# Kernel tuning notes

Hardware: AMD Instinct MI355X
Metric: run time of the kernel (lower is better)

Reference implementation:

```python
import jax, jax.numpy as jnp
import numpy as np

B, R, H, W = 128, 8, 256, 256


def _conv(x, w, b):
    # x: [1, C_in, h, w], w: [C_out, C_in, 3, 3]; stride 2, pad 1, then bias + ReLU
    y = jax.lax.conv_general_dilated(
        x, w, window_strides=(2, 2), padding=((1, 1), (1, 1)),
        dimension_numbers=('NCHW', 'OIHW', 'NCHW'))
    return jax.nn.relu(y + b[None, :, None, None])


def _single(x, w1, b1, w2, b2, w3, b3, fw, fb):
    # x: [3, H, W]; one sample through its region's CNN expert
    h = x[None]                      # [1,3,H,W]
    h = _conv(h, w1, b1)             # [1,32,H/2,W/2]
    h = _conv(h, w2, b2)             # [1,64,H/4,W/4]
    h = _conv(h, w3, b3)             # [1,128,H/8,W/8]
    feat = h.mean(axis=(2, 3))[0]    # [128] global average pool
    return fw @ feat + fb            # [num_classes]


def setup_inputs() -> dict:
    key = jax.random.key(0)
    ks = jax.random.split(key, 10)
    s = 0.05
    return {
        'image': jax.random.normal(ks[0], (B, 3, H, W), jnp.float32),
        'region': jax.random.randint(ks[1], (B,), 0, R, jnp.int64),
        'w1': jax.random.normal(ks[2], (R, 32, 3, 3, 3), jnp.float32) * s,
        'b1': jax.random.normal(ks[3], (R, 32), jnp.float32) * s,
        'w2': jax.random.normal(ks[4], (R, 64, 32, 3, 3), jnp.float32) * s,
        'b2': jax.random.normal(ks[5], (R, 64), jnp.float32) * s,
        'w3': jax.random.normal(ks[6], (R, 128, 64, 3, 3), jnp.float32) * s,
        'b3': jax.random.normal(ks[7], (R, 128), jnp.float32) * s,
        'fw': jax.random.normal(ks[8], (R, 2, 128), jnp.float32) * s,
        'fb': jax.random.normal(ks[9], (R, 2), jnp.float32) * s,
    }


def reference(image, region, w1, b1, w2, b2, w3, b3, fw, fb):
    # MoE-style dispatch: gather each sample's region weights, vmap per-sample expert.
    r = region.astype(jnp.int32)
    pw = [jnp.take(p, r, axis=0) for p in (w1, b1, w2, b2, w3, b3, fw, fb)]
    out = jax.vmap(_single)(image, *pw)  # [B, num_classes]
    return out
```

## Files before the change

kernel.cpp:

```cpp
#include <hip/hip_runtime.h>
#include <cstdint>


typedef __attribute__((ext_vector_type(8))) short short8;
typedef __attribute__((ext_vector_type(4))) float floatx4;
typedef __attribute__((ext_vector_type(4))) unsigned short ushort4v;
typedef __attribute__((ext_vector_type(4))) float float4v;

__device__ inline unsigned short f2bf(float f) {
  union { float f; unsigned u; } x;
  x.f = f;
  unsigned u = x.u;
  u += 0x7FFFu + ((u >> 16) & 1u);
  return (unsigned short)(u >> 16);
}

__device__ inline void g2l16(const unsigned short* g, unsigned short* l) {
  __builtin_amdgcn_global_load_lds(
      (const __attribute__((address_space(1))) unsigned int*)g,
      (__attribute__((address_space(3))) unsigned int*)(unsigned int)(uintptr_t)l,
      16, 0, 0);
}

__global__ __launch_bounds__(128) void prep_k(const int* __restrict__ rp,
                                              int* __restrict__ rout,
                                              float* __restrict__ feat) {
  __shared__ int is64;
  if (threadIdx.x == 0) {
    int odd_or = 0;
    for (int i = 0; i < 64; ++i) odd_or |= rp[2 * i + 1];
    is64 = (odd_or == 0) ? 1 : 0;
  }
  __syncthreads();
  int b = threadIdx.x;
  int r = is64 ? rp[2 * b] : rp[b];
  rout[b] = r & 7;
  float* fr = feat + b * 128;
  for (int j = 0; j < 128; ++j) fr[j] = 0.f;
}

__global__ __launch_bounds__(256) void pack1_k(const float* __restrict__ w,
                                               unsigned short* __restrict__ dst) {
  int t = blockIdx.x * blockDim.x + threadIdx.x;
  if (t >= 16384) return;
  int j = t & 7, lane = (t >> 3) & 63, mt = (t >> 9) & 1, kg = (t >> 10) & 1,
      r = t >> 11;
  int oc = mt * 16 + (lane & 15);
  int q = (lane >> 4) & 3;
  int row = kg * 2 + (q >> 1);
  int idx = (q & 1) * 8 + j;
  int kx = idx >> 2, c = idx & 3;
  float val = 0.f;
  if (row < 3 && kx < 3 && c < 3) val = w[((r * 32 + oc) * 3 + c) * 9 + row * 3 + kx];
  dst[t] = f2bf(val);
}

template <int OC, int IC, int SUBK, int MTG>
__global__ __launch_bounds__(256) void packT_k(const float* __restrict__ w,
                                               unsigned short* __restrict__ dst) {
  const int total = 8 * 9 * SUBK * MTG * 512;
  int t = blockIdx.x * blockDim.x + threadIdx.x;
  if (t >= total) return;
  int j = t & 7, lane = (t >> 3) & 63;
  int u = t >> 9;
  int mt = u % MTG; u /= MTG;
  int s = u % SUBK; u /= SUBK;
  int tap = u % 9;
  int r = u / 9;
  int oc = mt * 16 + (lane & 15);
  int ic = s * 32 + ((lane >> 4) & 3) * 8 + j;
  dst[t] = f2bf(w[((r * OC + oc) * IC + ic) * 9 + tap]);
}

__global__ __launch_bounds__(256) void halo8_k(unsigned short* __restrict__ buf,
                                               int nplane, int HP, int WP) {
  int per = 2 * WP + 2 * (HP - 2);
  int t = blockIdx.x * blockDim.x + threadIdx.x;
  if (t >= nplane * per) return;
  int s = t / per, i = t - s * per;
  int y, x;
  if (i < WP) { y = 0; x = i; }
  else if (i < 2 * WP) { y = HP - 1; x = i - WP; }
  else {
    int ii = i - 2 * WP;
    y = 1 + (ii >> 1);
    x = (ii & 1) ? (WP - 1) : 0;
  }
  short8 z = {0, 0, 0, 0, 0, 0, 0, 0};
  *(short8*)(buf + ((size_t)s * HP * WP + y * WP + x) * 8) = z;
}

__global__ __launch_bounds__(256, 3) void conv12_k(
    const float* __restrict__ img, const unsigned short* __restrict__ w1p,
    const float* __restrict__ b1, const unsigned short* __restrict__ w2p,
    const float* __restrict__ b2, const int* __restrict__ rgn,
    unsigned short* __restrict__ outp, int b0) {
  __shared__ unsigned short imgT[11 * 168 * 4];
  __shared__ unsigned short h1T[9 * 4 * 66 * 8];
  __shared__ float sB1[32];
  __shared__ float sB2[64];
  const int tid = threadIdx.x;
  const int xh = blockIdx.x;
  const int oy0 = blockIdx.y * 4;
  const int bl = blockIdx.z;
  const int r = __builtin_amdgcn_readfirstlane(rgn[b0 + bl]);
  if (tid < 32) sB1[tid] = b1[r * 32 + tid];
  if (tid >= 64 && tid < 128) sB2[tid - 64] = b2[r * 64 + (tid - 64)];
  const float* ib = img + (size_t)(b0 + bl) * 3 * 65536;
  const int padx = xh ? 65 : 0;
  const bool skiptop = (oy0 == 0);
  const int rb = xh * 128 - 4;

  const int n = tid & 15, q = (tid >> 4) & 3, wv = tid >> 6;
  const int lane = tid & 63;
  const short8* wpb1 = (const short8*)w1p + (size_t)r * 256 + lane;
  short8 afr1[2][2];
#pragma unroll
  for (int kg = 0; kg < 2; ++kg)
#pragma unroll
    for (int m = 0; m < 2; ++m) afr1[kg][m] = wpb1[(kg * 2 + m) * 64];

  auto STAGE = [&](int t0, int nrows) {
    const int nch = nrows * 41;
    for (int seg = 0; seg < nch; seg += 256) {
      int c = seg + tid;
      if (c < nch) {
        int i = c / 41, cq = c - i * 41;
        int rv = 4 * oy0 - 3 + t0 + i;
        int cb = rb + 4 * cq;
        unsigned short* dp = &imgT[((size_t)i * 168 + (4 * cq - 1)) * 4];
        if (rv >= 0 && cq > 0 && cb >= 0 && cb + 3 <= 255) {
          const float* p = ib + (size_t)rv * 256 + cb;
          float4v a = *(const float4v*)p;
          float4v bb = *(const float4v*)(p + 65536);
          float4v cc = *(const float4v*)(p + 131072);
#pragma unroll
          for (int e = 0; e < 4; ++e) {
            ushort4v v = {f2bf(a[e]), f2bf(bb[e]), f2bf(cc[e]), 0};
            *(ushort4v*)(dp + e * 4) = v;
          }
        } else {
          for (int e = (cq == 0 ? 1 : 0); e < 4; ++e) {
            int cc2 = cb + e;
            ushort4v v = {0, 0, 0, 0};
            if (rv >= 0 && cc2 >= 0 && cc2 <= 255) {
              const float* p = ib + (size_t)rv * 256 + cc2;
              v.x = f2bf(p[0]);
              v.y = f2bf(p[65536]);
              v.z = f2bf(p[131072]);
            }
            *(ushort4v*)(dp + e * 4) = v;
          }
        }
      }
    }
  };

  auto CONV1ROW = [&](int hy, int phaseB) {
    floatx4 a1[5][2];
#pragma unroll
    for (int nt = 0; nt < 5; ++nt)
#pragma unroll
      for (int m = 0; m < 2; ++m) a1[nt][m] = (floatx4){0.f, 0.f, 0.f, 0.f};
#pragma unroll
    for (int kg = 0; kg < 2; ++kg) {
      int row = kg * 2 + (q >> 1);
      int rowc = (row < 3) ? row : 0;
      int tr = 2 * hy + rowc;
      int slot = phaseB ? (tr >= 11 ? tr - 11 : tr) : tr;
#pragma unroll
      for (int nt = 0; nt < 5; ++nt) {
        int lx = nt * 16 + n;
        short8 bfr = *(const short8*)&imgT[((size_t)slot * 168 + 2 * lx) * 4 +
                                           (q & 1) * 8];
#pragma unroll
        for (int m = 0; m < 2; ++m)
          a1[nt][m] = __builtin_amdgcn_mfma_f32_16x16x32_bf16(
              afr1[kg][m], bfr, a1[nt][m], 0, 0, 0);
      }
    }
#pragma unroll
    for (int nt = 0; nt < 5; ++nt) {
      int lx = nt * 16 + n;
      bool ok = (lx <= 65) && (lx != padx) && !(skiptop && hy == 0);
      if (ok) {
#pragma unroll
        for (int m = 0; m < 2; ++m) {
          ushort4v st;
#pragma unroll
          for (int rr = 0; rr < 4; ++rr) {
            float v = a1[nt][m][rr] + sB1[m * 16 + q * 4 + rr];
            st[rr] = f2bf(v > 0.f ? v : 0.f);
          }
          int cg = m * 2 + (q >> 1);
          *(ushort4v*)&h1T[(((size_t)hy * 4 + cg) * 66 + lx) * 8 +
                           (q & 1) * 4] = st;
        }
      }
    }
  };

  STAGE(0, 11);
  {
    short8 z8 = {0, 0, 0, 0, 0, 0, 0, 0};
    if (tid < 36) {
      int hy = tid / 4, cg = tid % 4;
      *(short8*)&h1T[(((size_t)hy * 4 + cg) * 66 + padx) * 8] = z8;
    }
    if (skiptop) {
      for (int c = tid; c < 264; c += 256) {
        int cg = c / 66, x = c - cg * 66;
        *(short8*)&h1T[(((size_t)0 * 4 + cg) * 66 + x) * 8] = z8;
      }
    }
  }
  __syncthreads();

  for (int hy = wv; hy <= 4; hy += 4) CONV1ROW(hy, 0);
  __syncthreads();

  STAGE(11, 8);
  __syncthreads();

  CONV1ROW(5 + wv, 1);
  __syncthreads();

  const short8* wpb2 = (const short8*)w2p + (size_t)r * 9 * 4 * 64 + lane;
  floatx4 a2[2][4];
#pragma unroll
  for (int nt = 0; nt < 2; ++nt)
#pragma unroll
    for (int m = 0; m < 4; ++m) a2[nt][m] = (floatx4){0.f, 0.f, 0.f, 0.f};
#pragma unroll
  for (int tap = 0; tap < 9; ++tap) {
    const int ky = tap / 3, kx = tap % 3;
    short8 af[4];
#pragma unroll
    for (int m = 0; m < 4; ++m) af[m] = wpb2[(tap * 4 + m) * 64];
    short8 bf[2];
#pragma unroll
    for (int nt = 0; nt < 2; ++nt) {
      int ox = nt * 16 + n;
      bf[nt] = *(const short8*)&h1T[((((2 * wv + ky) << 2) + q) * 66 +
                                    (2 * ox + kx)) * 8];
    }
#pragma unroll
    for (int m = 0; m < 4; ++m)
#pragma unroll
      for (int nt = 0; nt < 2; ++nt)
        a2[nt][m] = __builtin_amdgcn_mfma_f32_16x16x32_bf16(af[m], bf[nt],
                                                            a2[nt][m], 0, 0, 0);
  }
  unsigned short* ob = outp + (size_t)bl * 8 * 66 * 66 * 8;
  const int oy = oy0 + wv;
#pragma unroll
  for (int nt = 0; nt < 2; ++nt) {
    int ox = xh * 32 + nt * 16 + n;
#pragma unroll
    for (int m = 0; m < 4; ++m) {
      ushort4v st;
#pragma unroll
      for (int rr = 0; rr < 4; ++rr) {
        float v = a2[nt][m][rr] + sB2[m * 16 + q * 4 + rr];
        st[rr] = f2bf(v > 0.f ? v : 0.f);
      }
      int cg = m * 2 + (q >> 1);
      *(ushort4v*)&ob[(((size_t)cg * 66 + oy + 1) * 66 + ox + 1) * 8 +
                      (q & 1) * 4] = st;
    }
  }
}

__global__ __launch_bounds__(128, 2) void conv3lds_k(
    const unsigned short* __restrict__ in, const unsigned short* __restrict__ wp,
    const float* __restrict__ bias, const int* __restrict__ rgn,
    float* __restrict__ feat, int b0) {
  __shared__ unsigned short tile[9 * 4 * 66 * 8];
  __shared__ float sBias[128];
  __shared__ float sGap[2 * 128];
  const int tid = threadIdx.x;
  const int bl = blockIdx.y;
  const int b = b0 + bl;
  const int r = __builtin_amdgcn_readfirstlane(rgn[b]);
  sBias[tid] = bias[r * 128 + tid];
  const int oy0 = blockIdx.x * 4;
  const unsigned short* gbase = in + (size_t)bl * 8 * 66 * 66 * 8;
  const int lane = tid & 63, wv = tid >> 6;
  const int n = lane & 15, q = (lane >> 4) & 3;
  const short8* wpb = (const short8*)wp + (size_t)r * 9 * 2 * 8 * 64 + lane;
  floatx4 acc[4][8];
#pragma unroll
  for (int nt = 0; nt < 4; ++nt)
#pragma unroll
    for (int m = 0; m < 8; ++m) acc[nt][m] = (floatx4){0.f, 0.f, 0.f, 0.f};
#pragma unroll
  for (int s = 0; s < 2; ++s) {
    __syncthreads();
    for (int seg = 0; seg < 2376; seg += 128) {
      int c = seg + tid;
      if (c < 2376) {
        int iy = c / 264;
        int rem = c - iy * 264;
        int c8 = rem / 66;
        int x = rem - c8 * 66;
        const unsigned short* gp =
            gbase + (((size_t)(s * 4 + c8) * 66 + 2 * oy0 + iy) * 66 + x) * 8;
        g2l16(gp, tile + (size_t)(seg + wv * 64) * 8);
      }
    }
    __syncthreads();
#pragma unroll
    for (int tap = 0; tap < 9; ++tap) {
      const int ky = tap / 3, kx = tap % 3;
      short8 afr[8];
#pragma unroll
      for (int m = 0; m < 8; ++m) afr[m] = wpb[((tap * 2 + s) * 8 + m) * 64];
      short8 bfr[4];
#pragma unroll
      for (int nt = 0; nt < 4; ++nt) {
        int oyl = 2 * wv + (nt >> 1);
        int ox = ((nt & 1) << 4) + n;
        bfr[nt] = *(const short8*)&tile[(((2 * oyl + ky) * 4 + q) * 66 +
                                        (2 * ox + kx)) * 8];
      }
#pragma unroll
      for (int m = 0; m < 8; ++m)
#pragma unroll
        for (int nt = 0; nt < 4; ++nt)
          acc[nt][m] = __builtin_amdgcn_mfma_f32_16x16x32_bf16(afr[m], bfr[nt],
                                                               acc[nt][m], 0, 0, 0);
    }
  }
#pragma unroll
  for (int m = 0; m < 8; ++m)
#pragma unroll
    for (int rr = 0; rr < 4; ++rr) {
      float bv = sBias[m * 16 + q * 4 + rr];
      float vs = 0.f;
#pragma unroll
      for (int nt = 0; nt < 4; ++nt) {
        float v = acc[nt][m][rr] + bv;
        vs += (v > 0.f ? v : 0.f);
      }
      vs += __shfl_xor(vs, 1, 16);
      vs += __shfl_xor(vs, 2, 16);
      vs += __shfl_xor(vs, 4, 16);
      vs += __shfl_xor(vs, 8, 16);
      if (n == 0) sGap[wv * 128 + m * 16 + q * 4 + rr] = vs;
    }
  __syncthreads();
  atomicAdd(&feat[b * 128 + tid], sGap[tid] + sGap[128 + tid]);
}

__global__ __launch_bounds__(256) void head_k(
    const float* __restrict__ feat, const float* __restrict__ fw,
    const float* __restrict__ fb, const int* __restrict__ rgn,
    float* __restrict__ out) {
  int t = threadIdx.x;
  int b = t >> 1, c = t & 1;
  int r = rgn[b];
  const float* fwr = fw + (r * 2 + c) * 128;
  const float* fv = feat + b * 128;
  float a = 0.f;
#pragma unroll 8
  for (int j = 0; j < 128; ++j) a = fmaf(fwr[j], fv[j], a);
  out[t] = a * (1.0f / 1024.0f) + fb[r * 2 + c];
}

extern "C" void kernel_launch(void* const* d_in, const int* in_sizes, int n_in,
                              void* d_out, int out_size, void* d_ws, size_t ws_size,
                              hipStream_t stream) {
  const float* img = (const float*)d_in[0];
  const int* rgn_raw = (const int*)d_in[1];
  const float* w1 = (const float*)d_in[2];
  const float* b1 = (const float*)d_in[3];
  const float* w2 = (const float*)d_in[4];
  const float* b2 = (const float*)d_in[5];
  const float* w3 = (const float*)d_in[6];
  const float* b3 = (const float*)d_in[7];
  const float* fw = (const float*)d_in[8];
  const float* fb = (const float*)d_in[9];
  float* out = (float*)d_out;

  const size_t h2p_s = (size_t)8 * 66 * 66 * 8 * 2;
  const size_t per_sample = h2p_s;
  const size_t fixed = (size_t)16384 * 2 + (size_t)147456 * 2 +
                       (size_t)589824 * 2 + 128 * 128 * 4 + 512 + 16 * 256;
  int C = 128;
  while (C > 1 && fixed + (size_t)C * per_sample > ws_size) C >>= 1;

  char* ws = (char*)d_ws;
  size_t off = 0;
  auto alloc = [&](size_t bytes) {
    char* p = ws + off;
    off += (bytes + 255) & ~(size_t)255;
    return p;
  };
  unsigned short* h2p = (unsigned short*)alloc((size_t)C * h2p_s);
  unsigned short* w1p = (unsigned short*)alloc((size_t)16384 * 2);
  unsigned short* w2p = (unsigned short*)alloc((size_t)147456 * 2);
  unsigned short* w3p = (unsigned short*)alloc((size_t)589824 * 2);
  float* feat = (float*)alloc((size_t)128 * 128 * 4);
  int* rgn = (int*)alloc((size_t)128 * 4);

  hipLaunchKernelGGL(prep_k, dim3(1), dim3(128), 0, stream, rgn_raw, rgn, feat);
  hipLaunchKernelGGL(pack1_k, dim3(64), dim3(256), 0, stream, w1, w1p);
  hipLaunchKernelGGL((packT_k<64, 32, 1, 4>), dim3(576), dim3(256), 0, stream, w2, w2p);
  hipLaunchKernelGGL((packT_k<128, 64, 2, 8>), dim3(2304), dim3(256), 0, stream, w3, w3p);
  {
    int n2 = C * 8 * (2 * 66 + 2 * 64);
    hipLaunchKernelGGL(halo8_k, dim3((n2 + 255) / 256), dim3(256), 0, stream,
                       h2p, C * 8, 66, 66);
  }

  for (int b0 = 0; b0 < 128; b0 += C) {
    hipLaunchKernelGGL(conv12_k, dim3(2, 16, C), dim3(256), 0, stream,
                       img, w1p, b1, w2p, b2, rgn, h2p, b0);
    hipLaunchKernelGGL(conv3lds_k, dim3(8, C), dim3(128), 0, stream,
                       h2p, w3p, b3, rgn, feat, b0);
  }
  hipLaunchKernelGGL(head_k, dim3(1), dim3(256), 0, stream, feat, fw, fb, rgn, out);
}
```

Before: 287.1 us.

## Merge setup kernels into one launch and widen conv3 to 4 waves

```diff
diff --git a/kernel.cpp b/kernel.cpp
--- a/kernel.cpp
+++ b/kernel.cpp
@@ -22,72 +22,79 @@
       16, 0, 0);
 }
 
-__global__ __launch_bounds__(128) void prep_k(const int* __restrict__ rp,
-                                              int* __restrict__ rout,
-                                              float* __restrict__ feat) {
-  __shared__ int is64;
-  if (threadIdx.x == 0) {
-    int odd_or = 0;
-    for (int i = 0; i < 64; ++i) odd_or |= rp[2 * i + 1];
-    is64 = (odd_or == 0) ? 1 : 0;
-  }
-  __syncthreads();
-  int b = threadIdx.x;
-  int r = is64 ? rp[2 * b] : rp[b];
-  rout[b] = r & 7;
-  float* fr = feat + b * 128;
-  for (int j = 0; j < 128; ++j) fr[j] = 0.f;
-}
-
-__global__ __launch_bounds__(256) void pack1_k(const float* __restrict__ w,
-                                               unsigned short* __restrict__ dst) {
-  int t = blockIdx.x * blockDim.x + threadIdx.x;
-  if (t >= 16384) return;
-  int j = t & 7, lane = (t >> 3) & 63, mt = (t >> 9) & 1, kg = (t >> 10) & 1,
-      r = t >> 11;
-  int oc = mt * 16 + (lane & 15);
-  int q = (lane >> 4) & 3;
-  int row = kg * 2 + (q >> 1);
-  int idx = (q & 1) * 8 + j;
-  int kx = idx >> 2, c = idx & 3;
-  float val = 0.f;
-  if (row < 3 && kx < 3 && c < 3) val = w[((r * 32 + oc) * 3 + c) * 9 + row * 3 + kx];
-  dst[t] = f2bf(val);
-}
-
-template <int OC, int IC, int SUBK, int MTG>
-__global__ __launch_bounds__(256) void packT_k(const float* __restrict__ w,
-                                               unsigned short* __restrict__ dst) {
-  const int total = 8 * 9 * SUBK * MTG * 512;
-  int t = blockIdx.x * blockDim.x + threadIdx.x;
-  if (t >= total) return;
-  int j = t & 7, lane = (t >> 3) & 63;
-  int u = t >> 9;
-  int mt = u % MTG; u /= MTG;
-  int s = u % SUBK; u /= SUBK;
-  int tap = u % 9;
-  int r = u / 9;
-  int oc = mt * 16 + (lane & 15);
-  int ic = s * 32 + ((lane >> 4) & 3) * 8 + j;
-  dst[t] = f2bf(w[((r * OC + oc) * IC + ic) * 9 + tap]);
-}
-
-__global__ __launch_bounds__(256) void halo8_k(unsigned short* __restrict__ buf,
-                                               int nplane, int HP, int WP) {
-  int per = 2 * WP + 2 * (HP - 2);
-  int t = blockIdx.x * blockDim.x + threadIdx.x;
-  if (t >= nplane * per) return;
-  int s = t / per, i = t - s * per;
-  int y, x;
-  if (i < WP) { y = 0; x = i; }
-  else if (i < 2 * WP) { y = HP - 1; x = i - WP; }
-  else {
-    int ii = i - 2 * WP;
-    y = 1 + (ii >> 1);
-    x = (ii & 1) ? (WP - 1) : 0;
-  }
-  short8 z = {0, 0, 0, 0, 0, 0, 0, 0};
-  *(short8*)(buf + ((size_t)s * HP * WP + y * WP + x) * 8) = z;
+__global__ __launch_bounds__(256) void setup_k(
+    const int* __restrict__ rp, int* __restrict__ rout, float* __restrict__ feat,
+    const float* __restrict__ w1, unsigned short* __restrict__ w1p,
+    const float* __restrict__ w2, unsigned short* __restrict__ w2p,
+    const float* __restrict__ w3, unsigned short* __restrict__ w3p,
+    unsigned short* __restrict__ h2p, int nhalo) {
+  const int tid = threadIdx.x;
+  if (blockIdx.x == 0) {
+    __shared__ int is64;
+    if (tid == 0) {
+      int odd_or = 0;
+      for (int i = 0; i < 64; ++i) odd_or |= rp[2 * i + 1];
+      is64 = (odd_or == 0) ? 1 : 0;
+    }
+    __syncthreads();
+    if (tid < 128) {
+      int r = is64 ? rp[2 * tid] : rp[tid];
+      rout[tid] = r & 7;
+      float* fr = feat + tid * 128;
+      for (int j = 0; j < 128; ++j) fr[j] = 0.f;
+    }
+    return;
+  }
+  int t = (blockIdx.x - 1) * 256 + tid;
+  if (t < 16384) {
+    int j = t & 7, lane = (t >> 3) & 63, mt = (t >> 9) & 1, kg = (t >> 10) & 1,
+        r = t >> 11;
+    int oc = mt * 16 + (lane & 15);
+    int q = (lane >> 4) & 3;
+    int row = kg * 2 + (q >> 1);
+    int idx = (q & 1) * 8 + j;
+    int kx = idx >> 2, c = idx & 3;
+    float val = 0.f;
+    if (row < 3 && kx < 3 && c < 3)
+      val = w1[((r * 32 + oc) * 3 + c) * 9 + row * 3 + kx];
+    w1p[t] = f2bf(val);
+  } else if (t < 163840) {
+    int t2 = t - 16384;
+    int j = t2 & 7, lane = (t2 >> 3) & 63;
+    int u = t2 >> 9;
+    int mt = u & 3; u >>= 2;
+    int tap = u % 9;
+    int r = u / 9;
+    int oc = mt * 16 + (lane & 15);
+    int ic = ((lane >> 4) & 3) * 8 + j;
+    w2p[t2] = f2bf(w2[((r * 64 + oc) * 32 + ic) * 9 + tap]);
+  } else if (t < 753664) {
+    int t3 = t - 163840;
+    int j = t3 & 7, lane = (t3 >> 3) & 63;
+    int u = t3 >> 9;
+    int mt = u & 7; u >>= 3;
+    int s = u & 1; u >>= 1;
+    int tap = u % 9;
+    int r = u / 9;
+    int oc = mt * 16 + (lane & 15);
+    int ic = s * 32 + ((lane >> 4) & 3) * 8 + j;
+    w3p[t3] = f2bf(w3[((r * 128 + oc) * 64 + ic) * 9 + tap]);
+  } else {
+    int th = t - 753664;
+    if (th < nhalo) {
+      int s = th / 260, i = th - s * 260;
+      int y, x;
+      if (i < 66) { y = 0; x = i; }
+      else if (i < 132) { y = 65; x = i - 66; }
+      else {
+        int ii = i - 132;
+        y = 1 + (ii >> 1);
+        x = (ii & 1) ? 65 : 0;
+      }
+      short8 z = {0, 0, 0, 0, 0, 0, 0, 0};
+      *(short8*)(h2p + ((size_t)s * 66 * 66 + y * 66 + x) * 8) = z;
+    }
+  }
 }
 
 __global__ __launch_bounds__(256, 3) void conv12_k(
@@ -271,66 +278,67 @@
   }
 }
 
-__global__ __launch_bounds__(128, 2) void conv3lds_k(
+__global__ __launch_bounds__(256, 2) void conv3f_k(
     const unsigned short* __restrict__ in, const unsigned short* __restrict__ wp,
     const float* __restrict__ bias, const int* __restrict__ rgn,
     float* __restrict__ feat, int b0) {
-  __shared__ unsigned short tile[9 * 4 * 66 * 8];
+  __shared__ unsigned short tile[9 * 8 * 66 * 8];
   __shared__ float sBias[128];
-  __shared__ float sGap[2 * 128];
+  __shared__ float sGap[4 * 128];
   const int tid = threadIdx.x;
   const int bl = blockIdx.y;
   const int b = b0 + bl;
   const int r = __builtin_amdgcn_readfirstlane(rgn[b]);
-  sBias[tid] = bias[r * 128 + tid];
+  if (tid < 128) sBias[tid] = bias[r * 128 + tid];
   const int oy0 = blockIdx.x * 4;
   const unsigned short* gbase = in + (size_t)bl * 8 * 66 * 66 * 8;
   const int lane = tid & 63, wv = tid >> 6;
   const int n = lane & 15, q = (lane >> 4) & 3;
+
+  for (int seg = 0; seg < 4752; seg += 256) {
+    int c = seg + tid;
+    if (c < 4752) {
+      int iy = c / 528;
+      int rem = c - iy * 528;
+      int c8 = rem / 66;
+      int x = rem - c8 * 66;
+      const unsigned short* gp =
+          gbase + (((size_t)c8 * 66 + 2 * oy0 + iy) * 66 + x) * 8;
+      g2l16(gp, tile + (size_t)(seg + wv * 64) * 8);
+    }
+  }
+  __syncthreads();
+
   const short8* wpb = (const short8*)wp + (size_t)r * 9 * 2 * 8 * 64 + lane;
-  floatx4 acc[4][8];
-#pragma unroll
-  for (int nt = 0; nt < 4; ++nt)
+  floatx4 acc[2][8];
+#pragma unroll
+  for (int nt = 0; nt < 2; ++nt)
 #pragma unroll
     for (int m = 0; m < 8; ++m) acc[nt][m] = (floatx4){0.f, 0.f, 0.f, 0.f};
-#pragma unroll
-  for (int s = 0; s < 2; ++s) {
-    __syncthreads();
-    for (int seg = 0; seg < 2376; seg += 128) {
-      int c = seg + tid;
-      if (c < 2376) {
-        int iy = c / 264;
-        int rem = c - iy * 264;
-        int c8 = rem / 66;
-        int x = rem - c8 * 66;
-        const unsigned short* gp =
-            gbase + (((size_t)(s * 4 + c8) * 66 + 2 * oy0 + iy) * 66 + x) * 8;
-        g2l16(gp, tile + (size_t)(seg + wv * 64) * 8);
-      }
-    }
-    __syncthreads();
+
+#pragma unroll
+  for (int s = 0; s < 2; ++s)
 #pragma unroll
     for (int tap = 0; tap < 9; ++tap) {
       const int ky = tap / 3, kx = tap % 3;
       short8 afr[8];
 #pragma unroll
       for (int m = 0; m < 8; ++m) afr[m] = wpb[((tap * 2 + s) * 8 + m) * 64];
-      short8 bfr[4];
-#pragma unroll
-      for (int nt = 0; nt < 4; ++nt) {
-        int oyl = 2 * wv + (nt >> 1);
-        int ox = ((nt & 1) << 4) + n;
-        bfr[nt] = *(const short8*)&tile[(((2 * oyl + ky) * 4 + q) * 66 +
+      short8 bfr[2];
+#pragma unroll
+      for (int nt = 0; nt < 2; ++nt) {
+        int ox = nt * 16 + n;
+        bfr[nt] = *(const short8*)&tile[((((2 * wv + ky) * 8) + s * 4 + q) * 66 +
                                         (2 * ox + kx)) * 8];
       }
 #pragma unroll
       for (int m = 0; m < 8; ++m)
 #pragma unroll
-        for (int nt = 0; nt < 4; ++nt)
+        for (int nt = 0; nt < 2; ++nt)
           acc[nt][m] = __builtin_amdgcn_mfma_f32_16x16x32_bf16(afr[m], bfr[nt],
                                                                acc[nt][m], 0, 0, 0);
     }
-  }
+
 #pragma unroll
   for (int m = 0; m < 8; ++m)
 #pragma unroll
@@ -338,7 +346,7 @@
       float bv = sBias[m * 16 + q * 4 + rr];
       float vs = 0.f;
 #pragma unroll
-      for (int nt = 0; nt < 4; ++nt) {
+      for (int nt = 0; nt < 2; ++nt) {
         float v = acc[nt][m][rr] + bv;
         vs += (v > 0.f ? v : 0.f);
       }
@@ -349,7 +357,9 @@
       if (n == 0) sGap[wv * 128 + m * 16 + q * 4 + rr] = vs;
     }
   __syncthreads();
-  atomicAdd(&feat[b * 128 + tid], sGap[tid] + sGap[128 + tid]);
+  if (tid < 128)
+    atomicAdd(&feat[b * 128 + tid],
+              sGap[tid] + sGap[128 + tid] + sGap[256 + tid] + sGap[384 + tid]);
 }
 
 __global__ __launch_bounds__(256) void head_k(
@@ -403,20 +413,18 @@
   float* feat = (float*)alloc((size_t)128 * 128 * 4);
   int* rgn = (int*)alloc((size_t)128 * 4);
 
-  hipLaunchKernelGGL(prep_k, dim3(1), dim3(128), 0, stream, rgn_raw, rgn, feat);
-  hipLaunchKernelGGL(pack1_k, dim3(64), dim3(256), 0, stream, w1, w1p);
-  hipLaunchKernelGGL((packT_k<64, 32, 1, 4>), dim3(576), dim3(256), 0, stream, w2, w2p);
-  hipLaunchKernelGGL((packT_k<128, 64, 2, 8>), dim3(2304), dim3(256), 0, stream, w3, w3p);
   {
-    int n2 = C * 8 * (2 * 66 + 2 * 64);
-    hipLaunchKernelGGL(halo8_k, dim3((n2 + 255) / 256), dim3(256), 0, stream,
-                       h2p, C * 8, 66, 66);
+    int nhalo = C * 8 * 260;
+    int total = 753664 + nhalo;
+    int nblk = 1 + (total + 255) / 256;
+    hipLaunchKernelGGL(setup_k, dim3(nblk), dim3(256), 0, stream,
+                       rgn_raw, rgn, feat, w1, w1p, w2, w2p, w3, w3p, h2p, nhalo);
   }
 
   for (int b0 = 0; b0 < 128; b0 += C) {
     hipLaunchKernelGGL(conv12_k, dim3(2, 16, C), dim3(256), 0, stream,
                        img, w1p, b1, w2p, b2, rgn, h2p, b0);
-    hipLaunchKernelGGL(conv3lds_k, dim3(8, C), dim3(128), 0, stream,
+    hipLaunchKernelGGL(conv3f_k, dim3(8, C), dim3(256), 0, stream,
                        h2p, w3p, b3, rgn, feat, b0);
   }
   hipLaunchKernelGGL(head_k, dim3(1), dim3(256), 0, stream, feat, fw, fb, rgn, out);
```

Measured after the change: 300.5 us. +4.7%, slower.
